# Kernel optimization log

Measured on AMD Instinct MI355X. Metric: run time of the kernel, lower is better.

Reference implementation:

```python
import jax, jax.numpy as jnp
import numpy as np
from jax import lax


def leaky(x):
    return jax.nn.leaky_relu(x, 0.01)


def masked_softmax(vec, mask, eps=1e-6):
    # softmax over entries where mask>0; zero elsewhere (stable via masked max)
    mask = mask.astype(vec.dtype)
    mx = jnp.max(jnp.where(mask > 0, vec, -jnp.inf), axis=1, keepdims=True)
    mx = jnp.where(jnp.isfinite(mx), mx, 0.0)
    e = jnp.exp(vec - mx) * mask
    return e / (e.sum(axis=1, keepdims=True) + eps)


def gru_dir(x, w_ih, w_hh, b_ih, b_hh, reverse):
    # PyTorch GRU cell math, one direction. x: [T, in]
    gi_all = x @ w_ih.T + b_ih  # [T, 3*GH], input gates precomputed
    def step(h, gi):
        gh = h @ w_hh.T + b_hh
        i_r, i_z, i_n = jnp.split(gi, 3)
        h_r, h_z, h_n = jnp.split(gh, 3)
        r = jax.nn.sigmoid(i_r + h_r)
        z = jax.nn.sigmoid(i_z + h_z)
        n = jnp.tanh(i_n + r * h_n)
        h2 = (1.0 - z) * n + z * h
        return h2, h2
    h0 = jnp.zeros((w_hh.shape[1],), x.dtype)
    _, ys = lax.scan(step, h0, gi_all, reverse=reverse)
    return ys  # [T, GH]


def setup_inputs():
    key = jax.random.key(0)
    ks = jax.random.split(key, 30)
    W, P, R, H = 128, 4096, 8192, 1024
    GH = H // 2
    s = 0.05
    def nrm(k, shp, sc):
        return jax.random.normal(k, shp, jnp.float32) * sc
    return {
        "word_feat": nrm(ks[0], (W, H), 1.0),
        "phrase_feat": nrm(ks[1], (P, H), 1.0),
        "rel_feat": nrm(ks[2], (R, H), 1.0),
        "w_ih_f": nrm(ks[3], (3 * GH, H), s), "w_hh_f": nrm(ks[4], (3 * GH, GH), s),
        "b_ih_f": nrm(ks[5], (3 * GH,), s), "b_hh_f": nrm(ks[6], (3 * GH,), s),
        "w_ih_b": nrm(ks[7], (3 * GH, H), s), "w_hh_b": nrm(ks[8], (3 * GH, GH), s),
        "b_ih_b": nrm(ks[9], (3 * GH,), s), "b_hh_b": nrm(ks[10], (3 * GH,), s),
        "w2p_w_W": nrm(ks[11], (H, H), s), "w2p_w_b": nrm(ks[12], (H,), s),
        "w2p_p_W": nrm(ks[13], (H, H), s), "w2p_p_b": nrm(ks[14], (H,), s),
        "w2p_t_W": nrm(ks[15], (H, H), s), "w2p_t_b": nrm(ks[16], (H,), s),
        "rel_W": nrm(ks[17], (H, 3 * H), s), "rel_b": nrm(ks[18], (H,), s),
        "att1_W": nrm(ks[19], (H, 4 * H), s), "att1_b": nrm(ks[20], (H,), s),
        "att2_W": nrm(ks[21], (1, H), s), "att2_b": nrm(ks[22], (1,), s),
        "r2p_t_W": nrm(ks[23], (H, H), s), "r2p_t_b": nrm(ks[24], (H,), s),
        "rel_conn_mat": jax.random.randint(ks[25], (2, R), 0, P),
        "word_to_graph_conn": jax.random.randint(ks[26], (P, W), 0, 2),
    }


def reference(word_feat, phrase_feat, rel_feat, w_ih_f, w_hh_f, b_ih_f, b_hh_f,
              w_ih_b, w_hh_b, b_ih_b, b_hh_b, w2p_w_W, w2p_w_b, w2p_p_W, w2p_p_b,
              w2p_t_W, w2p_t_b, rel_W, rel_b, att1_W, att1_b, att2_W, att2_b,
              r2p_t_W, r2p_t_b, rel_conn_mat, word_to_graph_conn):
    H = word_feat.shape[1]
    # bidirectional GRU over the word sequence
    lf = jnp.concatenate([
        gru_dir(word_feat, w_ih_f, w_hh_f, b_ih_f, b_hh_f, False),
        gru_dir(word_feat, w_ih_b, w_hh_b, b_ih_b, b_hh_b, True),
    ], axis=1)  # [T, H]
    ctx = jnp.concatenate([lf[0], lf[-1]])[None, :]  # [1, 2H]
    # word -> phrase attention
    a = (leaky(phrase_feat @ w2p_p_W.T + w2p_p_b)
         @ leaky(word_feat @ w2p_w_W.T + w2p_w_b).T) / jnp.sqrt(jnp.float32(H))
    a = masked_softmax(a, word_to_graph_conn)
    upd = phrase_feat + (a @ word_feat) @ w2p_t_W.T + w2p_t_b  # [P, H]
    # phrase -> rel
    sub, obj = rel_conn_mat[0], rel_conn_mat[1]
    Rn = sub.shape[0]
    Pn = upd.shape[0]
    urel = jnp.concatenate([upd[sub], upd[obj], rel_feat], 1) @ rel_W.T + rel_b  # [R, H]
    # rel -> phrase with sparse connectivity (each rel touches subject+object)
    ar = jnp.arange(Rn)
    mask = jnp.zeros((Pn, Rn), upd.dtype).at[sub, ar].set(1.0).at[obj, ar].set(1.0)
    ix = jnp.concatenate([sub, obj])
    iy = jnp.concatenate([ar, ar])
    fuse = jnp.concatenate(
        [upd[ix], urel[iy], jnp.broadcast_to(ctx, (ix.shape[0], ctx.shape[1]))], 1)  # [2R, 4H]
    s = (leaky(fuse @ att1_W.T + att1_b) @ att2_W.T + att2_b)[:, 0]
    att = jnp.zeros((Pn, Rn), upd.dtype).at[ix, iy].set(s)
    att = masked_softmax(att, mask)
    out_phrase = upd + (att @ urel) @ r2p_t_W.T + r2p_t_b
    return (word_feat, out_phrase, urel)
```

## Files before the change

kernel.cpp:

```cpp
#include <hip/hip_runtime.h>

#define DEV __device__ __forceinline__

typedef short s16x8 __attribute__((ext_vector_type(8)));
typedef float f32x4 __attribute__((ext_vector_type(4)));
typedef __fp16 fp16x8 __attribute__((ext_vector_type(8)));
typedef unsigned short u16;
typedef unsigned long long u64;

constexpr int Wn = 128;
constexpr int Pn = 4096;
constexpr int Rn = 8192;
constexpr int Hn = 1024;

DEV float b2f(u16 u) { union { unsigned i; float f; } x; x.i = (unsigned)u << 16; return x.f; }
DEV u16 f2b(float f) {
  union { float f; unsigned i; } x; x.f = f;
  unsigned r = x.i + 0x7FFF + ((x.i >> 16) & 1);
  return (u16)(r >> 16);
}
DEV u16 f2h(float x) { __fp16 h = (__fp16)x; u16 r; __builtin_memcpy(&r, &h, 2); return r; }
DEV float leaky(float x) { return x >= 0.f ? x : 0.01f * x; }

DEV void load_lds16(const void* g, void* l) {
  __builtin_amdgcn_global_load_lds(
      (const __attribute__((address_space(1))) void*)g,
      (__attribute__((address_space(3))) void*)l, 16, 0, 0);
}

DEV float wred_sum(float v) {
  #pragma unroll
  for (int m = 1; m < 64; m <<= 1) v += __shfl_xor(v, m, 64);
  return v;
}
DEV float wred_max(float v) {
  #pragma unroll
  for (int m = 1; m < 64; m <<= 1) v = fmaxf(v, __shfl_xor(v, m, 64));
  return v;
}

template<bool OUTF32, bool ACT, bool BIAS, bool RES, bool DUAL>
DEV void gemm_tile(char* sm,
    const u16* __restrict__ A, int lda, const u16* __restrict__ B, int ldb,
    void* Cp, int ldc, const float* __restrict__ bias,
    const float* res, int ldr, u16* C16, float alpha, int K, int m0, int n0)
{
  char* As = sm;
  char* Bs = sm + 16384;
  const int tid = threadIdx.x;
  const int lane = tid & 63, w = tid >> 6;
  const int wr = (w >> 1) * 64, wc = (w & 1) * 64;
  const int r_lo = lane & 15, kq = lane >> 4;

  __syncthreads();

  f32x4 acc[4][4];
  #pragma unroll
  for (int i = 0; i < 4; ++i)
    #pragma unroll
    for (int j = 0; j < 4; ++j) acc[i][j] = (f32x4){0.f, 0.f, 0.f, 0.f};

  for (int kt = 0; kt < K; kt += 64) {
    if (kt) __syncthreads();
    #pragma unroll
    for (int i = 0; i < 4; ++i) {
      int f = i * 4096 + tid * 16;
      int row = f >> 7, colb = f & 127;
      int scol = colb ^ ((row & 7) << 4);
      load_lds16((const char*)(A + (size_t)(m0 + row) * lda + kt) + scol,
                 As + i * 4096 + w * 1024);
    }
    #pragma unroll
    for (int i = 0; i < 4; ++i) {
      int f = i * 4096 + tid * 16;
      int row = f >> 7, colb = f & 127;
      int scol = colb ^ ((row & 7) << 4);
      load_lds16((const char*)(B + (size_t)(n0 + row) * ldb + kt) + scol,
                 Bs + i * 4096 + w * 1024);
    }
    __syncthreads();
    #pragma unroll
    for (int ks = 0; ks < 2; ++ks) {
      s16x8 af[4], bfr[4];
      const int kb = ks * 64 + kq * 16;
      #pragma unroll
      for (int mi = 0; mi < 4; ++mi) {
        int row = wr + mi * 16 + r_lo;
        af[mi] = *(const s16x8*)(As + row * 128 + (kb ^ ((row & 7) << 4)));
      }
      #pragma unroll
      for (int ni = 0; ni < 4; ++ni) {
        int row = wc + ni * 16 + r_lo;
        bfr[ni] = *(const s16x8*)(Bs + row * 128 + (kb ^ ((row & 7) << 4)));
      }
      #pragma unroll
      for (int mi = 0; mi < 4; ++mi)
        #pragma unroll
        for (int ni = 0; ni < 4; ++ni)
          acc[mi][ni] = __builtin_amdgcn_mfma_f32_16x16x32_bf16(af[mi], bfr[ni], acc[mi][ni], 0, 0, 0);
    }
  }
  #pragma unroll
  for (int mi = 0; mi < 4; ++mi)
    #pragma unroll
    for (int ni = 0; ni < 4; ++ni)
      #pragma unroll
      for (int j = 0; j < 4; ++j) {
        int r = m0 + wr + mi * 16 + kq * 4 + j;
        int c = n0 + wc + ni * 16 + r_lo;
        float v = acc[mi][ni][j] * alpha;
        if (BIAS) v += bias[c];
        if (RES)  v += res[(size_t)r * ldr + c];
        if (ACT)  v = leaky(v);
        if (OUTF32) ((float*)Cp)[(size_t)r * ldc + c] = v;
        else        ((u16*)Cp)[(size_t)r * ldc + c] = f2b(v);
        if (DUAL)   C16[(size_t)r * ldc + c] = f2b(v);
      }
}

template<bool OUTF32, bool ACT, bool BIAS, bool RES, bool DUAL>
__global__ __launch_bounds__(256) void k_gemm_bt(
    const u16* __restrict__ A, int lda, const u16* __restrict__ B, int ldb,
    void* Cp, int ldc, const float* __restrict__ bias,
    const float* res, int ldr, u16* C16, float alpha, int K)
{
  __shared__ __align__(16) char sm[32768];
  gemm_tile<OUTF32, ACT, BIAS, RES, DUAL>(sm, A, lda, B, ldb, Cp, ldc, bias,
      res, ldr, C16, alpha, K, blockIdx.y * 128, blockIdx.x * 128);
}

__global__ __launch_bounds__(256) void k_gemm_af32(
    const float* __restrict__ A, int lda, const u16* __restrict__ B, int ldb,
    u16* __restrict__ C, int ldc, int K)
{
  __shared__ __align__(16) char sm[32768];
  char* As = sm;
  char* Bs = sm + 16384;
  const int tid = threadIdx.x;
  const int lane = tid & 63, w = tid >> 6;
  const int m0 = blockIdx.y * 128, n0 = blockIdx.x * 128;
  const int wr = (w >> 1) * 64, wc = (w & 1) * 64;
  const int r_lo = lane & 15, kq = lane >> 4;

  f32x4 acc[4][4];
  #pragma unroll
  for (int i = 0; i < 4; ++i)
    #pragma unroll
    for (int j = 0; j < 4; ++j) acc[i][j] = (f32x4){0.f, 0.f, 0.f, 0.f};

  for (int kt = 0; kt < K; kt += 64) {
    if (kt) __syncthreads();
    #pragma unroll
    for (int i = 0; i < 4; ++i) {
      int e = i * 2048 + tid * 8;
      int row = e >> 6, col = e & 63;
      const float* s = A + (size_t)(m0 + row) * lda + kt + col;
      float4 a4 = *(const float4*)s;
      float4 b4 = *(const float4*)(s + 4);
      u16 d8[8] = {f2b(a4.x), f2b(a4.y), f2b(a4.z), f2b(a4.w),
                   f2b(b4.x), f2b(b4.y), f2b(b4.z), f2b(b4.w)};
      int byte = (col * 2) ^ ((row & 7) << 4);
      *(uint4*)(As + row * 128 + byte) = *(uint4*)d8;
    }
    #pragma unroll
    for (int i = 0; i < 4; ++i) {
      int f = i * 4096 + tid * 16;
      int row = f >> 7, colb = f & 127;
      int scol = colb ^ ((row & 7) << 4);
      load_lds16((const char*)(B + (size_t)(n0 + row) * ldb + kt) + scol,
                 Bs + i * 4096 + w * 1024);
    }
    __syncthreads();
    #pragma unroll
    for (int ks = 0; ks < 2; ++ks) {
      s16x8 af[4], bfr[4];
      const int kb = ks * 64 + kq * 16;
      #pragma unroll
      for (int mi = 0; mi < 4; ++mi) {
        int row = wr + mi * 16 + r_lo;
        af[mi] = *(const s16x8*)(As + row * 128 + (kb ^ ((row & 7) << 4)));
      }
      #pragma unroll
      for (int ni = 0; ni < 4; ++ni) {
        int row = wc + ni * 16 + r_lo;
        bfr[ni] = *(const s16x8*)(Bs + row * 128 + (kb ^ ((row & 7) << 4)));
      }
      #pragma unroll
      for (int mi = 0; mi < 4; ++mi)
        #pragma unroll
        for (int ni = 0; ni < 4; ++ni)
          acc[mi][ni] = __builtin_amdgcn_mfma_f32_16x16x32_bf16(af[mi], bfr[ni], acc[mi][ni], 0, 0, 0);
    }
  }
  #pragma unroll
  for (int mi = 0; mi < 4; ++mi)
    #pragma unroll
    for (int ni = 0; ni < 4; ++ni)
      #pragma unroll
      for (int j = 0; j < 4; ++j) {
        int r = m0 + wr + mi * 16 + kq * 4 + j;
        int c = n0 + wc + ni * 16 + r_lo;
        C[(size_t)r * ldc + c] = f2b(acc[mi][ni][j]);
      }
}

__global__ __launch_bounds__(256) void k_rf3(
    const u16* __restrict__ G, const u16* __restrict__ relU,
    const u16* __restrict__ W3s, const float* __restrict__ rel_b,
    float* __restrict__ out_urel)
{
  __shared__ __align__(16) char sm[32768];
  int half = blockIdx.y >> 5;
  gemm_tile<true, false, true, false, false>(sm,
      half ? relU : G, Hn, W3s, Hn,
      out_urel + (size_t)half * 4096 * Hn, Hn, rel_b, nullptr, 0, nullptr,
      1.f, Hn, (blockIdx.y & 31) * 128, blockIdx.x * 128);
}

__global__ __launch_bounds__(256) void k_gemm_rel(
    const u16* __restrict__ upd16, const int* __restrict__ rcm,
    const u16* __restrict__ W1, const u16* __restrict__ W2,
    float* __restrict__ out_urel)
{
  __shared__ __align__(16) char sm[32768];
  __shared__ int ridx[2][128];
  char* As = sm;
  char* Bs = sm + 16384;
  const int tid = threadIdx.x;
  const int lane = tid & 63, w = tid >> 6;
  const int hh = blockIdx.y >> 5;
  const int m0 = (blockIdx.y & 31) * 128, n0 = blockIdx.x * 128;
  const int wr = (w >> 1) * 64, wc = (w & 1) * 64;
  const int r_lo = lane & 15, kq = lane >> 4;
  const int* sub = rcm + hh * 4096;
  const int* obj = rcm + Rn + hh * 4096;
  float* C = out_urel + (size_t)hh * 4096 * Hn;

  if (tid < 128) ridx[0][tid] = sub[m0 + tid];
  else ridx[1][tid - 128] = obj[m0 + tid - 128];
  __syncthreads();

  f32x4 acc[4][4];
  #pragma unroll
  for (int i = 0; i < 4; ++i)
    #pragma unroll
    for (int j = 0; j < 4; ++j) acc[i][j] = (f32x4){0.f, 0.f, 0.f, 0.f};

  for (int kt = 0; kt < 2048; kt += 64) {
    const int half = kt >> 10;
    const int kk = kt & 1023;
    const u16* Wm = half ? W2 : W1;
    __syncthreads();
    #pragma unroll
    for (int i = 0; i < 4; ++i) {
      int f = i * 4096 + tid * 16;
      int row = f >> 7, colb = f & 127;
      int scol = colb ^ ((row & 7) << 4);
      load_lds16((const char*)(upd16 + (size_t)ridx[half][row] * 1024 + kk) + scol,
                 As + i * 4096 + w * 1024);
    }
    #pragma unroll
    for (int i = 0; i < 4; ++i) {
      int f = i * 4096 + tid * 16;
      int row = f >> 7, colb = f & 127;
      int scol = colb ^ ((row & 7) << 4);
      load_lds16((const char*)(Wm + (size_t)(n0 + row) * 1024 + kk) + scol,
                 Bs + i * 4096 + w * 1024);
    }
    __syncthreads();
    #pragma unroll
    for (int ks = 0; ks < 2; ++ks) {
      s16x8 af[4], bfr[4];
      const int kb = ks * 64 + kq * 16;
      #pragma unroll
      for (int mi = 0; mi < 4; ++mi) {
        int row = wr + mi * 16 + r_lo;
        af[mi] = *(const s16x8*)(As + row * 128 + (kb ^ ((row & 7) << 4)));
      }
      #pragma unroll
      for (int ni = 0; ni < 4; ++ni) {
        int row = wc + ni * 16 + r_lo;
        bfr[ni] = *(const s16x8*)(Bs + row * 128 + (kb ^ ((row & 7) << 4)));
      }
      #pragma unroll
      for (int mi = 0; mi < 4; ++mi)
        #pragma unroll
        for (int ni = 0; ni < 4; ++ni)
          acc[mi][ni] = __builtin_amdgcn_mfma_f32_16x16x32_bf16(af[mi], bfr[ni], acc[mi][ni], 0, 0, 0);
    }
  }
  #pragma unroll
  for (int mi = 0; mi < 4; ++mi)
    #pragma unroll
    for (int ni = 0; ni < 4; ++ni)
      #pragma unroll
      for (int j = 0; j < 4; ++j) {
        int r = m0 + wr + mi * 16 + kq * 4 + j;
        int c = n0 + wc + ni * 16 + r_lo;
        C[(size_t)r * Hn + c] = acc[mi][ni][j] + C[(size_t)r * Hn + c];
      }
}

struct CvtTask { const float* src; u16* dst; int sld; int units; };
struct MKArgs {
  const float *w_hh_f, *w_hh_b, *b_hh_f, *b_hh_b;
  const float *word_feat, *w_ih_f, *w_ih_b, *b_ih_f, *b_ih_b;
  const float *phrase_feat, *w2p_w_b, *w2p_p_b, *w2p_t_b;
  const int *rcm, *conn;
  float *gi_f, *gi_b, *scores, *out_phr, *ctx;
  u16 *wf16, *wih16f, *wih16b, *wl;
  u16 *pf16, *w2pw16, *w2pp16, *w2pt16, *pl, *attw, *wfT, *aw, *upd16;
  u64* X; int* pc; int* cnt2; int* offs; int* cursor;
  CvtTask t[12]; int nt;
};

__global__ __launch_bounds__(256) void k_mega(MKArgs a)
{
  __shared__ __align__(16) u16 wlds[96 * 512];
  __shared__ float bh[96];
  __shared__ float partg[4][96];
  __shared__ __align__(16) u16 hb[512];

  const int bid = blockIdx.x;
  const int tid = threadIdx.x;
  const int lane = tid & 63, wv = tid >> 6;
  const int NW = (int)gridDim.x - 32;

  if (bid >= 32) {
    const int bc = bid - 32, nb = NW;
    int bar = 0;
    auto wbarrier = [&]() {
      __syncthreads();
      if (tid == 0) {
        __hip_atomic_fetch_add(&a.pc[bar], 1, __ATOMIC_ACQ_REL, __HIP_MEMORY_SCOPE_AGENT);
        while (__hip_atomic_load(&a.pc[bar], __ATOMIC_ACQUIRE, __HIP_MEMORY_SCOPE_AGENT) < NW)
          __builtin_amdgcn_s_sleep(4);
      }
      __syncthreads();
      ++bar;
    };
    auto cvt_task = [&](const float* src, int sld, u16* dst, int units) {
      for (int u = bc * 256 + tid; u < units; u += nb * 256) {
        int row = u >> 7, c = (u & 127) * 8;
        const float* s = src + (size_t)row * sld + c;
        float4 va = *(const float4*)s;
        float4 vb = *(const float4*)(s + 4);
        ushort4 lo = {f2b(va.x), f2b(va.y), f2b(va.z), f2b(va.w)};
        ushort4 hi = {f2b(vb.x), f2b(vb.y), f2b(vb.z), f2b(vb.w)};
        *(ushort4*)(dst + (size_t)row * 1024 + c) = lo;
        *(ushort4*)(dst + (size_t)row * 1024 + c + 4) = hi;
      }
    };

    cvt_task(a.word_feat, Hn, a.wf16, Wn * 128);
    cvt_task(a.w_ih_f, Hn, a.wih16f, 1536 * 128);
    cvt_task(a.w_ih_b, Hn, a.wih16b, 1536 * 128);
    wbarrier();
    for (int u = bc; u < 24; u += nb) {
      const u16* Bm = u < 12 ? a.wih16f : a.wih16b;
      float* Cm = u < 12 ? a.gi_f : a.gi_b;
      const float* bm = u < 12 ? a.b_ih_f : a.b_ih_b;
      gemm_tile<true, false, true, false, false>((char*)wlds, a.wf16, Hn, Bm, Hn,
          Cm, 1536, bm, nullptr, 0, nullptr, 1.f, Hn, 0, (u % 12) * 128);
    }
    for (int u = bc * 256 + tid; u < 2 * Rn; u += nb * 256) {
      if (u < Rn && a.rcm[u] == a.rcm[Rn + u]) continue;
      atomicAdd(a.cnt2 + a.rcm[u], 1);
    }
    wbarrier();
    if (bc == 0) {
      int* part = (int*)wlds;
      int* pscan = part + 256;
      int loc[16]; int s = 0;
      #pragma unroll
      for (int i = 0; i < 16; ++i) { loc[i] = a.cnt2[tid * 16 + i]; s += loc[i]; }
      part[tid] = s; __syncthreads();
      if (tid == 0) { int acc = 0; for (int i = 0; i < 256; ++i) { pscan[i] = acc; acc += part[i]; } }
      __syncthreads();
      int base = pscan[tid];
      #pragma unroll
      for (int i = 0; i < 16; ++i) {
        a.offs[tid * 16 + i] = base; a.cursor[tid * 16 + i] = base; base += loc[i];
      }
      if (tid == 255) a.offs[Pn] = base;
      __syncthreads();
    }
    for (int k = 0; k < a.nt; ++k)
      cvt_task(a.t[k].src, a.t[k].sld, a.t[k].dst, a.t[k].units);
    wbarrier();
    for (int u = bc; u < 264; u += nb) {
      if (u < 8)
        gemm_tile<false, true, true, false, false>((char*)wlds, a.wf16, Hn,
            a.w2pw16, Hn, a.wl, Hn, a.w2p_w_b, nullptr, 0, nullptr, 1.f, Hn,
            0, u * 128);
      else {
        int t2 = u - 8;
        gemm_tile<false, true, true, false, false>((char*)wlds, a.pf16, Hn,
            a.w2pp16, Hn, a.pl, Hn, a.w2p_p_b, nullptr, 0, nullptr, 1.f, Hn,
            (t2 >> 3) * 128, (t2 & 7) * 128);
      }
    }
    wbarrier();
    for (int u = bc; u < 544; u += nb) {
      if (u < 32)
        gemm_tile<true, false, false, false, false>((char*)wlds, a.pl, Hn,
            a.wl, Hn, a.scores, Wn, nullptr, nullptr, 0, nullptr, 0.03125f, Hn,
            u * 128, 0);
      else {
        int idx = (u - 32) * 256 + tid;
        int r = idx >> 10, c = idx & 1023;
        a.wfT[c * 128 + r] = a.wf16[idx];
      }
    }
    wbarrier();
    for (int u = bc; u < 1024; u += nb) {
      int p = u * 4 + wv;
      float v0 = a.scores[(size_t)p * 128 + lane];
      float v1 = a.scores[(size_t)p * 128 + 64 + lane];
      int m0 = a.conn[(size_t)p * 128 + lane];
      int m1 = a.conn[(size_t)p * 128 + 64 + lane];
      float x0 = m0 > 0 ? v0 : -INFINITY;
      float x1 = m1 > 0 ? v1 : -INFINITY;
      float mx = wred_max(fmaxf(x0, x1));
      if (!(mx > -INFINITY)) mx = 0.f;
      float e0 = m0 > 0 ? __expf(v0 - mx) : 0.f;
      float e1 = m1 > 0 ? __expf(v1 - mx) : 0.f;
      float s = wred_sum(e0 + e1);
      float inv = 1.f / (s + 1e-6f);
      a.attw[(size_t)p * 128 + lane] = f2b(e0 * inv);
      a.attw[(size_t)p * 128 + 64 + lane] = f2b(e1 * inv);
    }
    wbarrier();
    for (int u = bc; u < 256; u += nb)
      gemm_tile<false, false, false, false, false>((char*)wlds, a.attw, Wn,
          a.wfT, Wn, a.aw, Hn, nullptr, nullptr, 0, nullptr, 1.f, Wn,
          (u >> 3) * 128, (u & 7) * 128);
    wbarrier();
    for (int u = bc; u < 256; u += nb)
      gemm_tile<true, false, true, true, true>((char*)wlds, a.aw, Hn,
          a.w2pt16, Hn, a.out_phr, Hn, a.w2p_t_b, a.phrase_feat, Hn, a.upd16,
          1.f, Hn, (u >> 3) * 128, (u & 7) * 128);
    return;
  }

  const int dir = bid >> 4;
  const int b   = bid & 15;
  const float* w_hh = dir ? a.w_hh_b : a.w_hh_f;
  const float* b_hhp = dir ? a.b_hh_b : a.b_hh_f;
  const float* gi = dir ? a.gi_b : a.gi_f;
  u64* Xd = a.X + (size_t)dir * 128 * 256;

  for (int idx = tid; idx < 96 * 128; idx += 256) {
    int gl = idx >> 7;
    int kc = (idx & 127) << 2;
    int g  = 32 * b + (gl & 31) + ((gl >> 5) << 9);
    float4 wv4 = *(const float4*)(w_hh + (size_t)g * 512 + kc);
    u16 d4[4] = {f2h(wv4.x), f2h(wv4.y), f2h(wv4.z), f2h(wv4.w)};
    int byte = (kc * 2) ^ ((gl & 7) << 4);
    *(uint2*)((char*)wlds + gl * 1024 + byte) = *(uint2*)d4;
  }
  if (tid < 96) {
    int g = 32 * b + (tid & 31) + ((tid >> 5) << 9);
    bh[tid] = b_hhp[g];
  }
  for (int i = tid; i < 256; i += 256) ((unsigned*)hb)[i] = 0u;
  if (tid == 0) {
    while (__hip_atomic_load(&a.pc[1], __ATOMIC_ACQUIRE, __HIP_MEMORY_SCOPE_AGENT) < NW)
      __builtin_amdgcn_s_sleep(16);
  }
  __syncthreads();

  float hprev = 0.f;
  const int jg = 32 * b + tid;
  const int r_lo = lane & 15, kq = lane >> 4;
  const fp16x8 zf = {0, 0, 0, 0, 0, 0, 0, 0};

  for (int sidx = 0; sidx < 128; ++sidx) {
    const int t = dir ? (127 - sidx) : sidx;

    float gir = 0.f, giz = 0.f, gin = 0.f;
    if (tid < 32) {
      gir = gi[t * 1536 + jg];
      giz = gi[t * 1536 + 512 + jg];
      gin = gi[t * 1536 + 1024 + jg];
    }

    f32x4 acc6[6];
    #pragma unroll
    for (int gt = 0; gt < 6; ++gt) acc6[gt] = (f32x4){0.f, 0.f, 0.f, 0.f};
    #pragma unroll
    for (int k2 = 0; k2 < 4; ++k2) {
      int kt = (wv << 2) + k2;
      fp16x8 bf = (r_lo == 0) ? *(const fp16x8*)(hb + kt * 32 + kq * 8) : zf;
      #pragma unroll
      for (int gt = 0; gt < 6; ++gt) {
        int gl = gt * 16 + r_lo;
        int byte = (kt * 64 + kq * 16) ^ ((gl & 7) << 4);
        fp16x8 af = *(const fp16x8*)((const char*)wlds + gl * 1024 + byte);
        acc6[gt] = __builtin_amdgcn_mfma_f32_16x16x32_f16(af, bf, acc6[gt], 0, 0, 0);
      }
    }
    if (r_lo == 0) {
      #pragma unroll
      for (int gt = 0; gt < 6; ++gt)
        #pragma unroll
        for (int j = 0; j < 4; ++j)
          partg[wv][gt * 16 + kq * 4 + j] = acc6[gt][j];
    }
    __syncthreads();

    if (wv == 0) {
      float h2v = 0.f;
      if (lane < 32) {
        int j = lane;
        float ghr = partg[0][j] + partg[1][j] + partg[2][j] + partg[3][j] + bh[j];
        float ghz = partg[0][j + 32] + partg[1][j + 32] + partg[2][j + 32] + partg[3][j + 32] + bh[j + 32];
        float ghn = partg[0][j + 64] + partg[1][j + 64] + partg[2][j + 64] + partg[3][j + 64] + bh[j + 64];
        float rr = 1.f / (1.f + __expf(-(gir + ghr)));
        float zz = 1.f / (1.f + __expf(-(giz + ghz)));
        float nn = tanhf(gin + rr * ghn);
        h2v = (1.f - zz) * nn + zz * hprev;
        hprev = h2v;
        if (sidx == 0)   a.ctx[(dir ? 1536 : 0)    + jg] = h2v;
        if (sidx == 127) a.ctx[(dir ? 512  : 1024) + jg] = h2v;
      }
      if (sidx < 127) {
        float q0 = __shfl(h2v, (lane & 15) * 2, 64);
        float q1 = __shfl(h2v, (lane & 15) * 2 + 1, 64);
        if (lane < 16) {
          u64 pk = (u64)f2h(q0) | ((u64)f2h(q1) << 16) |
                   ((u64)(unsigned)(sidx + 1) << 32);
          __hip_atomic_store(&Xd[(size_t)sidx * 256 + b * 16 + lane], pk,
                             __ATOMIC_RELAXED, __HIP_MEMORY_SCOPE_AGENT);
        }
        const u64* src = Xd + (size_t)sidx * 256;
        const unsigned want = (unsigned)(sidx + 1);
        const int base = lane * 4;
        u64 v[4];
        unsigned done = 0;
        while (done != 0xFu) {
          #pragma unroll
          for (int i = 0; i < 4; ++i)
            if (!(done & (1u << i)))
              v[i] = __hip_atomic_load(&src[base + i], __ATOMIC_RELAXED,
                                       __HIP_MEMORY_SCOPE_AGENT);
          #pragma unroll
          for (int i = 0; i < 4; ++i)
            if (!(done & (1u << i)) && (unsigned)(v[i] >> 32) == want)
              done |= 1u << i;
          if (done != 0xFu) __builtin_amdgcn_s_sleep(1);
        }
        #pragma unroll
        for (int i = 0; i < 4; ++i)
          ((unsigned*)hb)[base + i] = (unsigned)v[i];
      }
    }
    __syncthreads();
  }
}

__global__ __launch_bounds__(256) void k_cvec(const float* __restrict__ att1W,
    const float* __restrict__ att1b, const float* __restrict__ ctx, float* __restrict__ cvec)
{
  int i = blockIdx.x * 4 + (threadIdx.x >> 6);
  int lane = threadIdx.x & 63;
  const float* wrow = att1W + (size_t)i * 4096 + 2048 + lane * 32;
  const float* cp = ctx + lane * 32;
  float acc = 0.f;
  #pragma unroll
  for (int k = 0; k < 32; ++k) acc += wrow[k] * cp[k];
  acc = wred_sum(acc);
  if (lane == 0) cvec[i] = acc + att1b[i];
}

__global__ __launch_bounds__(256) void k_edge_s(const int* __restrict__ rcm,
    const u16* __restrict__ U1, const u16* __restrict__ V1, const float* __restrict__ cvec,
    const float* __restrict__ att2w, const float* __restrict__ att2b,
    float* __restrict__ sval)
{
  int idx = blockIdx.x * 4 + (threadIdx.x >> 6);
  int lane = threadIdx.x & 63;
  int rL = idx < Rn ? idx : idx - Rn;
  int p = rcm[idx];
  const u16* u = U1 + (size_t)p * Hn + lane * 16;
  const u16* v = V1 + (size_t)rL * Hn + lane * 16;
  const float* aw = att2w + lane * 16;
  const float* cv = cvec + lane * 16;
  float acc = 0.f;
  #pragma unroll
  for (int i = 0; i < 16; ++i) {
    float x = b2f(u[i]) + b2f(v[i]) + cv[i];
    acc += aw[i] * leaky(x);
  }
  acc = wred_sum(acc);
  if (lane == 0) sval[idx] = acc + att2b[0];
}

__global__ __launch_bounds__(256) void k_fill(const int* __restrict__ rcm,
    const float* __restrict__ sval, int* __restrict__ cursor,
    int* __restrict__ er, float* __restrict__ es)
{
  int e = blockIdx.x * 256 + threadIdx.x;
  if (e < Rn && rcm[e] == rcm[Rn + e]) return;
  int slot = atomicAdd(cursor + rcm[e], 1);
  er[slot] = e & (Rn - 1);
  es[slot] = sval[e];
}

__global__ __launch_bounds__(256) void k_att_apply(const int* __restrict__ offs,
    const int* __restrict__ er, const float* __restrict__ es,
    const float* __restrict__ urel, u16* __restrict__ pacc)
{
  int p = blockIdx.x;
  int tid = threadIdx.x;
  int beg = offs[p], end = offs[p + 1];
  float mx = -INFINITY;
  for (int i = beg; i < end; ++i) mx = fmaxf(mx, es[i]);
  float den = 1e-6f;
  for (int i = beg; i < end; ++i) den += __expf(es[i] - mx);
  float inv = 1.f / den;
  float a0 = 0.f, a1 = 0.f, a2 = 0.f, a3 = 0.f;
  int c0 = tid * 4;
  for (int i = beg; i < end; ++i) {
    float wgt = __expf(es[i] - mx) * inv;
    float4 q = *(const float4*)(urel + (size_t)er[i] * Hn + c0);
    a0 += wgt * q.x; a1 += wgt * q.y; a2 += wgt * q.z; a3 += wgt * q.w;
  }
  ushort4 ov; ov.x = f2b(a0); ov.y = f2b(a1); ov.z = f2b(a2); ov.w = f2b(a3);
  *(ushort4*)(pacc + (size_t)p * Hn + c0) = ov;
}

extern "C" void kernel_launch(void* const* d_in, const int* in_sizes, int n_in,
                              void* d_out, int out_size, void* d_ws, size_t ws_size,
                              hipStream_t stream)
{
  const float* word_feat   = (const float*)d_in[0];
  const float* phrase_feat = (const float*)d_in[1];
  const float* rel_feat    = (const float*)d_in[2];
  const float* w_ih_f = (const float*)d_in[3];
  const float* w_hh_f = (const float*)d_in[4];
  const float* b_ih_f = (const float*)d_in[5];
  const float* b_hh_f = (const float*)d_in[6];
  const float* w_ih_b = (const float*)d_in[7];
  const float* w_hh_b = (const float*)d_in[8];
  const float* b_ih_b = (const float*)d_in[9];
  const float* b_hh_b = (const float*)d_in[10];
  const float* w2p_w_W = (const float*)d_in[11];
  const float* w2p_w_b = (const float*)d_in[12];
  const float* w2p_p_W = (const float*)d_in[13];
  const float* w2p_p_b = (const float*)d_in[14];
  const float* w2p_t_W = (const float*)d_in[15];
  const float* w2p_t_b = (const float*)d_in[16];
  const float* rel_W   = (const float*)d_in[17];
  const float* rel_b   = (const float*)d_in[18];
  const float* att1_W  = (const float*)d_in[19];
  const float* att1_b  = (const float*)d_in[20];
  const float* att2_W  = (const float*)d_in[21];
  const float* att2_b  = (const float*)d_in[22];
  const float* r2p_t_W = (const float*)d_in[23];
  const float* r2p_t_b = (const float*)d_in[24];
  const int* rcm  = (const int*)d_in[25];
  const int* conn = (const int*)d_in[26];

  float* out_word = (float*)d_out;
  float* out_phr  = out_word + (size_t)Wn * Hn;
  float* out_urel = out_phr + (size_t)Pn * Hn;

  char* ws = (char*)d_ws;
  size_t off = 0;
  auto alloc = [&](size_t bytes) -> char* {
    char* pptr = ws + off; off += (bytes + 255) & ~(size_t)255; return pptr;
  };
  int*   cnt2   = (int*)alloc(Pn * 4);
  int*   pc     = (int*)alloc(64 * 4);
  u64*   X      = (u64*)alloc(2 * 128 * 256 * 8);
  size_t zlen   = (size_t)((char*)(X + 2 * 128 * 256) - (char*)cnt2);
  float* ctx    = (float*)alloc(2048 * 4);
  float* cvec   = (float*)alloc(1024 * 4);
  int*   cursor = (int*)alloc(Pn * 4);
  int*   offs   = (int*)alloc((Pn + 1) * 4);
  int*   er     = (int*)alloc(2 * Rn * 4);
  float* es     = (float*)alloc(2 * Rn * 4);
  float* sval   = (float*)alloc(2 * Rn * 4);
  float* gi_f   = (float*)alloc(128 * 1536 * 4);
  float* gi_b   = (float*)alloc(128 * 1536 * 4);
  u16*   wf16   = (u16*)alloc((size_t)Wn * Hn * 2);
  u16*   wl     = (u16*)alloc((size_t)Wn * Hn * 2);
  u16*   upd16  = (u16*)alloc((size_t)Pn * Hn * 2);
  char*  RA     = alloc(16777216);
  u16*   W1s    = (u16*)RA;
  u16*   W2s    = (u16*)(RA + 2097152);
  u16*   W3s    = (u16*)(RA + 4194304);
  u16*   G      = (u16*)(RA + 6291456);
  u16*   V1f    = (u16*)RA;
  u16*   A1p16  = (u16*)alloc(2097152);
  u16*   A1r16  = (u16*)alloc(2097152);
  u16*   U1     = (u16*)alloc((size_t)Pn * Hn * 2);
  u16*   relU16 = U1;
  u16*   r2pW16 = (u16*)alloc(2097152);
  u16*   pacc   = upd16;

  char* phrB = (char*)out_phr;
  u16*   wih16f = (u16*)phrB;
  u16*   wih16b = (u16*)(phrB + 3145728);
  float* scores = (float*)(phrB + 6291456);
  char* urlB = (char*)out_urel;
  u16*   pf16   = (u16*)urlB;
  u16*   w2pw16 = (u16*)(urlB + 8388608);
  u16*   w2pp16 = (u16*)(urlB + 10485760);
  u16*   w2pt16 = (u16*)(urlB + 12582912);
  u16*   pl     = (u16*)(urlB + 14680064);
  u16*   aw     = (u16*)(urlB + 23068672);
  u16*   attw   = (u16*)(urlB + 31457280);
  u16*   wfT    = (u16*)(urlB + 32505856);

  (void)hipMemsetAsync(cnt2, 0, zlen, stream);

  dim3 blk(256);

  MKArgs A;
  A.w_hh_f = w_hh_f; A.w_hh_b = w_hh_b; A.b_hh_f = b_hh_f; A.b_hh_b = b_hh_b;
  A.word_feat = word_feat; A.w_ih_f = w_ih_f; A.w_ih_b = w_ih_b;
  A.b_ih_f = b_ih_f; A.b_ih_b = b_ih_b;
  A.phrase_feat = phrase_feat; A.w2p_w_b = w2p_w_b; A.w2p_p_b = w2p_p_b;
  A.w2p_t_b = w2p_t_b; A.rcm = rcm; A.conn = conn;
  A.gi_f = gi_f; A.gi_b = gi_b; A.scores = scores; A.out_phr = out_phr; A.ctx = ctx;
  A.wf16 = wf16; A.wih16f = wih16f; A.wih16b = wih16b; A.wl = wl;
  A.pf16 = pf16; A.w2pw16 = w2pw16; A.w2pp16 = w2pp16; A.w2pt16 = w2pt16;
  A.pl = pl; A.attw = attw; A.wfT = wfT; A.aw = aw; A.upd16 = upd16;
  A.X = X; A.pc = pc; A.cnt2 = cnt2; A.offs = offs; A.cursor = cursor;
  A.t[0]  = {phrase_feat,    pf16,   Hn,     Pn * 128};
  A.t[1]  = {w2p_w_W,        w2pw16, Hn,     1024 * 128};
  A.t[2]  = {w2p_p_W,        w2pp16, Hn,     1024 * 128};
  A.t[3]  = {w2p_t_W,        w2pt16, Hn,     1024 * 128};
  A.t[4]  = {rel_W,          W1s,    3 * Hn, 1024 * 128};
  A.t[5]  = {rel_W + Hn,     W2s,    3 * Hn, 1024 * 128};
  A.t[6]  = {rel_W + 2 * Hn, W3s,    3 * Hn, 1024 * 128};
  A.t[7]  = {att1_W,         A1p16,  4 * Hn, 1024 * 128};
  A.t[8]  = {att1_W + Hn,    A1r16,  4 * Hn, 1024 * 128};
  A.t[9]  = {r2p_t_W,        r2pW16, Hn,     1024 * 128};
  A.t[10] = {rel_feat,       G,      Hn,     4096 * 128};
  A.t[11] = {rel_feat + (size_t)4096 * Hn, relU16, Hn, 4096 * 128};
  A.nt = 12;
  k_mega<<<256, blk, 0, stream>>>(A);
  k_cvec<<<256, blk, 0, stream>>>(att1_W, att1_b, ctx, cvec);

  k_rf3<<<dim3(8, 64), blk, 0, stream>>>(G, relU16, W3s, rel_b, out_urel);
  k_gemm_rel<<<dim3(8, 64), blk, 0, stream>>>(upd16, rcm, W1s, W2s, out_urel);

  k_gemm_bt<false, false, false, false, false><<<dim3(8, 32), blk, 0, stream>>>(
      upd16, Hn, A1p16, Hn, U1, Hn, nullptr, nullptr, 0, nullptr, 1.f, Hn);
  k_gemm_af32<<<dim3(8, 64), blk, 0, stream>>>(
      out_urel, Hn, A1r16, Hn, V1f, Hn, Hn);

  k_edge_s<<<(2 * Rn) / 4, blk, 0, stream>>>(rcm, U1, V1f, cvec, att2_W, att2_b, sval);
  k_fill<<<(2 * Rn) / 256, blk, 0, stream>>>(rcm, sval, cursor, er, es);
  k_att_apply<<<Pn, blk, 0, stream>>>(offs, er, es, out_urel, pacc);
  k_gemm_bt<true, false, true, true, false><<<dim3(8, 32), blk, 0, stream>>>(
      pacc, Hn, r2pW16, Hn, out_phr, Hn, r2p_t_b, out_phr, Hn, nullptr, 1.f, Hn);

  (void)hipMemcpyAsync(out_word, word_feat, (size_t)Wn * Hn * 4,
                       hipMemcpyDeviceToDevice, stream);
}
```

Measured before the change: 736.9 us.

## Start GRU recurrence earlier by fusing w_ih conversion into gi GEMM and dedicated counter

The input-gate GEMM now reads fp32 w_ih directly and converts it to bf16 while loading LDS tiles, which removes the separate conversion pass. Each of the 24 gi tiles bumps a dedicated counter, so the GRU scan blocks can begin once gi is ready instead of waiting on the first full worker barrier. The bulk weight conversions are merged into the first barrier phase, and the w2p_t GEMM moves out of the mega kernel into a separate launch. Combined, these shorten the critical path ahead of the serial GRU. The cost is an extra kernel launch and repeated fp32 B loads with in-loop conversion.

```diff
diff --git a/kernel.cpp b/kernel.cpp
--- a/kernel.cpp
+++ b/kernel.cpp
@@ -127,6 +127,82 @@
   __shared__ __align__(16) char sm[32768];
   gemm_tile<OUTF32, ACT, BIAS, RES, DUAL>(sm, A, lda, B, ldb, Cp, ldc, bias,
       res, ldr, C16, alpha, K, blockIdx.y * 128, blockIdx.x * 128);
+}
+
+DEV void gemm_tile_bf32(char* sm,
+    const u16* __restrict__ A, int lda, const float* __restrict__ Bf, int ldb,
+    float* __restrict__ C, int ldc, const float* __restrict__ bias,
+    int K, int m0, int n0)
+{
+  char* As = sm;
+  char* Bs = sm + 16384;
+  const int tid = threadIdx.x;
+  const int lane = tid & 63, w = tid >> 6;
+  const int wr = (w >> 1) * 64, wc = (w & 1) * 64;
+  const int r_lo = lane & 15, kq = lane >> 4;
+
+  __syncthreads();
+
+  f32x4 acc[4][4];
+  #pragma unroll
+  for (int i = 0; i < 4; ++i)
+    #pragma unroll
+    for (int j = 0; j < 4; ++j) acc[i][j] = (f32x4){0.f, 0.f, 0.f, 0.f};
+
+  for (int kt = 0; kt < K; kt += 64) {
+    if (kt) __syncthreads();
+    #pragma unroll
+    for (int i = 0; i < 4; ++i) {
+      int f = i * 4096 + tid * 16;
+      int row = f >> 7, colb = f & 127;
+      int scol = colb ^ ((row & 7) << 4);
+      load_lds16((const char*)(A + (size_t)(m0 + row) * lda + kt) + scol,
+                 As + i * 4096 + w * 1024);
+    }
+    #pragma unroll
+    for (int i = 0; i < 4; ++i) {
+      int e = i * 2048 + tid * 8;
+      int row = e >> 6, col = e & 63;
+      const float* s = Bf + (size_t)(n0 + row) * ldb + kt + col;
+      float4 a4 = *(const float4*)s;
+      float4 b4 = *(const float4*)(s + 4);
+      u16 d8[8] = {f2b(a4.x), f2b(a4.y), f2b(a4.z), f2b(a4.w),
+                   f2b(b4.x), f2b(b4.y), f2b(b4.z), f2b(b4.w)};
+      int byte = (col * 2) ^ ((row & 7) << 4);
+      *(uint4*)(Bs + row * 128 + byte) = *(uint4*)d8;
+    }
+    __syncthreads();
+    #pragma unroll
+    for (int ks = 0; ks < 2; ++ks) {
+      s16x8 af[4], bfr[4];
+      const int kb = ks * 64 + kq * 16;
+      #pragma unroll
+      for (int mi = 0; mi < 4; ++mi) {
+        int row = wr + mi * 16 + r_lo;
+        af[mi] = *(const s16x8*)(As + row * 128 + (kb ^ ((row & 7) << 4)));
+      }
+      #pragma unroll
+      for (int ni = 0; ni < 4; ++ni) {
+        int row = wc + ni * 16 + r_lo;
+        bfr[ni] = *(const s16x8*)(Bs + row * 128 + (kb ^ ((row & 7) << 4)));
+      }
+      #pragma unroll
+      for (int mi = 0; mi < 4; ++mi)
+        #pragma unroll
+        for (int ni = 0; ni < 4; ++ni)
+          acc[mi][ni] = __builtin_amdgcn_mfma_f32_16x16x32_bf16(af[mi], bfr[ni], acc[mi][ni], 0, 0, 0);
+    }
+  }
+  #pragma unroll
+  for (int mi = 0; mi < 4; ++mi)
+    #pragma unroll
+    for (int ni = 0; ni < 4; ++ni)
+      #pragma unroll
+      for (int j = 0; j < 4; ++j) {
+        int r = m0 + wr + mi * 16 + kq * 4 + j;
+        int c = n0 + wc + ni * 16 + r_lo;
+        C[(size_t)r * ldc + c] = acc[mi][ni][j] + bias[c];
+      }
 }
 
 __global__ __launch_bounds__(256) void k_gemm_af32(
@@ -305,11 +381,10 @@
 struct MKArgs {
   const float *w_hh_f, *w_hh_b, *b_hh_f, *b_hh_b;
   const float *word_feat, *w_ih_f, *w_ih_b, *b_ih_f, *b_ih_b;
-  const float *phrase_feat, *w2p_w_b, *w2p_p_b, *w2p_t_b;
+  const float *w2p_w_b, *w2p_p_b;
   const int *rcm, *conn;
-  float *gi_f, *gi_b, *scores, *out_phr, *ctx;
-  u16 *wf16, *wih16f, *wih16b, *wl;
-  u16 *pf16, *w2pw16, *w2pp16, *w2pt16, *pl, *attw, *wfT, *aw, *upd16;
+  float *gi_f, *gi_b, *scores, *ctx;
+  u16 *wf16, *wl, *pf16, *w2pw16, *w2pp16, *pl, *attw, *wfT, *aw;
   u64* X; int* pc; int* cnt2; int* offs; int* cursor;
   CvtTask t[12]; int nt;
 };
@@ -353,20 +428,23 @@
     };
 
     cvt_task(a.word_feat, Hn, a.wf16, Wn * 128);
-    cvt_task(a.w_ih_f, Hn, a.wih16f, 1536 * 128);
-    cvt_task(a.w_ih_b, Hn, a.wih16b, 1536 * 128);
     wbarrier();
-    for (int u = bc; u < 24; u += nb) {
-      const u16* Bm = u < 12 ? a.wih16f : a.wih16b;
-      float* Cm = u < 12 ? a.gi_f : a.gi_b;
-      const float* bm = u < 12 ? a.b_ih_f : a.b_ih_b;
-      gemm_tile<true, false, true, false, false>((char*)wlds, a.wf16, Hn, Bm, Hn,
-          Cm, 1536, bm, nullptr, 0, nullptr, 1.f, Hn, 0, (u % 12) * 128);
+    if (bc < 24) {
+      const float* Bm = bc < 12 ? a.w_ih_f : a.w_ih_b;
+      float* Cm = bc < 12 ? a.gi_f : a.gi_b;
+      const float* bm = bc < 12 ? a.b_ih_f : a.b_ih_b;
+      gemm_tile_bf32((char*)wlds, a.wf16, Hn, Bm, Hn, Cm, 1536, bm, Hn,
+                     0, (bc % 12) * 128);
+      __syncthreads();
+      if (tid == 0)
+        __hip_atomic_fetch_add(&a.pc[32], 1, __ATOMIC_ACQ_REL, __HIP_MEMORY_SCOPE_AGENT);
     }
     for (int u = bc * 256 + tid; u < 2 * Rn; u += nb * 256) {
       if (u < Rn && a.rcm[u] == a.rcm[Rn + u]) continue;
       atomicAdd(a.cnt2 + a.rcm[u], 1);
     }
+    for (int k = 0; k < a.nt; ++k)
+      cvt_task(a.t[k].src, a.t[k].sld, a.t[k].dst, a.t[k].units);
     wbarrier();
     if (bc == 0) {
       int* part = (int*)wlds;
@@ -385,9 +463,6 @@
       if (tid == 255) a.offs[Pn] = base;
       __syncthreads();
     }
-    for (int k = 0; k < a.nt; ++k)
-      cvt_task(a.t[k].src, a.t[k].sld, a.t[k].dst, a.t[k].units);
-    wbarrier();
     for (int u = bc; u < 264; u += nb) {
       if (u < 8)
         gemm_tile<false, true, true, false, false>((char*)wlds, a.wf16, Hn,
@@ -435,11 +510,6 @@
       gemm_tile<false, false, false, false, false>((char*)wlds, a.attw, Wn,
           a.wfT, Wn, a.aw, Hn, nullptr, nullptr, 0, nullptr, 1.f, Wn,
           (u >> 3) * 128, (u & 7) * 128);
-    wbarrier();
-    for (int u = bc; u < 256; u += nb)
-      gemm_tile<true, false, true, true, true>((char*)wlds, a.aw, Hn,
-          a.w2pt16, Hn, a.out_phr, Hn, a.w2p_t_b, a.phrase_feat, Hn, a.upd16,
-          1.f, Hn, (u >> 3) * 128, (u & 7) * 128);
     return;
   }
 
@@ -465,8 +535,8 @@
   }
   for (int i = tid; i < 256; i += 256) ((unsigned*)hb)[i] = 0u;
   if (tid == 0) {
-    while (__hip_atomic_load(&a.pc[1], __ATOMIC_ACQUIRE, __HIP_MEMORY_SCOPE_AGENT) < NW)
-      __builtin_amdgcn_s_sleep(16);
+    while (__hip_atomic_load(&a.pc[32], __ATOMIC_ACQUIRE, __HIP_MEMORY_SCOPE_AGENT) < 24)
+      __builtin_amdgcn_s_sleep(8);
   }
   __syncthreads();
 
@@ -700,10 +770,7 @@
   u16*   r2pW16 = (u16*)alloc(2097152);
   u16*   pacc   = upd16;
 
-  char* phrB = (char*)out_phr;
-  u16*   wih16f = (u16*)phrB;
-  u16*   wih16b = (u16*)(phrB + 3145728);
-  float* scores = (float*)(phrB + 6291456);
+  float* scores = (float*)out_phr;
   char* urlB = (char*)out_urel;
   u16*   pf16   = (u16*)urlB;
   u16*   w2pw16 = (u16*)(urlB + 8388608);
@@ -722,12 +789,12 @@
   A.w_hh_f = w_hh_f; A.w_hh_b = w_hh_b; A.b_hh_f = b_hh_f; A.b_hh_b = b_hh_b;
   A.word_feat = word_feat; A.w_ih_f = w_ih_f; A.w_ih_b = w_ih_b;
   A.b_ih_f = b_ih_f; A.b_ih_b = b_ih_b;
-  A.phrase_feat = phrase_feat; A.w2p_w_b = w2p_w_b; A.w2p_p_b = w2p_p_b;
-  A.w2p_t_b = w2p_t_b; A.rcm = rcm; A.conn = conn;
-  A.gi_f = gi_f; A.gi_b = gi_b; A.scores = scores; A.out_phr = out_phr; A.ctx = ctx;
-  A.wf16 = wf16; A.wih16f = wih16f; A.wih16b = wih16b; A.wl = wl;
-  A.pf16 = pf16; A.w2pw16 = w2pw16; A.w2pp16 = w2pp16; A.w2pt16 = w2pt16;
-  A.pl = pl; A.attw = attw; A.wfT = wfT; A.aw = aw; A.upd16 = upd16;
+  A.w2p_w_b = w2p_w_b; A.w2p_p_b = w2p_p_b;
+  A.rcm = rcm; A.conn = conn;
+  A.gi_f = gi_f; A.gi_b = gi_b; A.scores = scores; A.ctx = ctx;
+  A.wf16 = wf16; A.wl = wl;
+  A.pf16 = pf16; A.w2pw16 = w2pw16; A.w2pp16 = w2pp16;
+  A.pl = pl; A.attw = attw; A.wfT = wfT; A.aw = aw;
   A.X = X; A.pc = pc; A.cnt2 = cnt2; A.offs = offs; A.cursor = cursor;
   A.t[0]  = {phrase_feat,    pf16,   Hn,     Pn * 128};
   A.t[1]  = {w2p_w_W,        w2pw16, Hn,     1024 * 128};
@@ -745,6 +812,9 @@
   k_mega<<<256, blk, 0, stream>>>(A);
   k_cvec<<<256, blk, 0, stream>>>(att1_W, att1_b, ctx, cvec);
 
+  k_gemm_bt<true, false, true, true, true><<<dim3(8, 32), blk, 0, stream>>>(
+      aw, Hn, w2pt16, Hn, out_phr, Hn, w2p_t_b, phrase_feat, Hn, upd16, 1.f, Hn);
+
   k_rf3<<<dim3(8, 64), blk, 0, stream>>>(G, relU16, W3s, rel_b, out_urel);
   k_gemm_rel<<<dim3(8, 64), blk, 0, stream>>>(upd16, rcm, W1s, W2s, out_urel);
 
```

New measurement: 764.6 us. +3.8%, slower.
